# Kernel optimization log

Measured on AMD Instinct MI355X. Metric: run time of the kernel, lower is better.

The kernel has to match this reference:

```python
import jax, jax.numpy as jnp
import numpy as np

LN_EPS = 1e-12


def setup_inputs() -> dict:
    key = jax.random.key(0)
    k1, k2, k3, k4 = jax.random.split(key, 4)
    B, H, L, D = 2, 12, 2048, 64
    q = jax.random.normal(k1, (B, H, L, D), dtype=jnp.float32)
    k = jax.random.normal(k2, (B, H, L, D), dtype=jnp.float32)
    v = jax.random.normal(k3, (B, H, L, D), dtype=jnp.float32)
    mask = jax.random.randint(k4, (1, 1, L, L), 0, 2).astype(jnp.int32)
    gamma = jnp.ones((D,), dtype=jnp.float32)
    beta = jnp.zeros((D,), dtype=jnp.float32)
    return {"q": q, "k": k, "v": v, "mask": mask, "gamma": gamma, "beta": beta}


def reference(q, k, v, mask, gamma, beta):
    # score = q @ k^T  -> [B, H, L, L]
    score = jnp.einsum("bhqd,bhkd->bhqk", q, k)
    # masked_fill(mask == 0, -10000)
    score = jnp.where(mask == 0, jnp.float32(-10000.0), score)
    # result = score @ v -> [B, H, L, D]  (no softmax)
    result = jnp.einsum("bhqk,bhkd->bhqd", score, v)
    # layer norm over the last dim (d_tensor)
    mean = jnp.mean(result, axis=-1, keepdims=True)
    var = jnp.var(result, axis=-1, keepdims=True)
    normed = (result - mean) / jnp.sqrt(var + LN_EPS)
    return normed * gamma + beta
```

## Files before the change

kernel.cpp:

```cpp
#include <hip/hip_runtime.h>

#define SEQ 2048
#define HD 64
#define NBH 24

#define MB_OFF   0
#define MB_BYTES (32 * 32 * 512)
#define QB_OFF   (MB_OFF + MB_BYTES)
#define QK_BYTES (NBH * SEQ * HD * 2)
#define KB_OFF   (QB_OFF + QK_BYTES)
#define VT_OFF   (KB_OFF + QK_BYTES)
#define WS_NEED  ((size_t)(VT_OFF + QK_BYTES))

typedef __bf16 bfrag8 __attribute__((ext_vector_type(8)));
typedef __bf16 bf16x4 __attribute__((ext_vector_type(4)));
typedef float  floatx4 __attribute__((ext_vector_type(4)));
typedef float  floatx16 __attribute__((ext_vector_type(16)));

__device__ __forceinline__ floatx4 mfma_16x16x32(bfrag8 a, bfrag8 b, floatx4 c) {
    return __builtin_amdgcn_mfma_f32_16x16x32_bf16(a, b, c, 0, 0, 0);
}
__device__ __forceinline__ floatx16 mfma_32x32x16(bfrag8 a, bfrag8 b, floatx16 c) {
    return __builtin_amdgcn_mfma_f32_32x32x16_bf16(a, b, c, 0, 0, 0);
}
__device__ __forceinline__ void gld16(const unsigned char* g, unsigned char* l) {
    __builtin_amdgcn_global_load_lds(
        (const __attribute__((address_space(1))) unsigned int*)g,
        (__attribute__((address_space(3))) unsigned int*)l, 16, 0, 0);
}

__global__ __launch_bounds__(256)
void prep_kernel(const float* __restrict__ qp, const float* __restrict__ kp,
                 const float* __restrict__ vp, const int* __restrict__ maskp,
                 unsigned char* __restrict__ ws)
{
    __shared__ __attribute__((aligned(16))) unsigned char parena[64 * 68 * 4];
    const int t = threadIdx.x;
    const int b = blockIdx.x;

    if (b < 1536) {
        int gt  = b * 256 + t;
        int row = gt >> 3;
        int c   = gt & 7;
        const floatx4* qs = (const floatx4*)(qp + row * 64 + c * 8);
        const floatx4* ks = (const floatx4*)(kp + row * 64 + c * 8);
        floatx4 q0 = qs[0], q1 = qs[1];
        floatx4 k0 = ks[0], k1 = ks[1];
        bfrag8 qpk, kpk;
        #pragma unroll
        for (int i = 0; i < 4; ++i) {
            qpk[i] = (__bf16)q0[i]; qpk[4 + i] = (__bf16)q1[i];
            kpk[i] = (__bf16)k0[i]; kpk[4 + i] = (__bf16)k1[i];
        }
        *(bfrag8*)(ws + QB_OFF + row * 128 + c * 16) = qpk;
        *(bfrag8*)(ws + KB_OFF + row * 128 + ((c ^ (row & 7)) * 16)) = kpk;
    } else if (b < 2304) {
        int bb = b - 1536, bh = bb >> 5, kt = bb & 31;
        float* lf = (float*)parena;
        const floatx4* vg = (const floatx4*)(vp + (bh * SEQ + kt * 64) * 64);
        #pragma unroll
        for (int it = 0; it < 4; ++it) {
            int f = t + it * 256;
            int r = f >> 4, c4 = f & 15;
            floatx4 val = vg[f];
            #pragma unroll
            for (int i = 0; i < 4; ++i) lf[r * 68 + c4 * 4 + i] = val[i];
        }
        __syncthreads();
        int d = t >> 2, kseg = t & 3;
        unsigned char* tb = ws + VT_OFF + (size_t)(bh * 32 + kt) * 8192 + d * 128;
        #pragma unroll
        for (int jj = 0; jj < 2; ++jj) {
            bfrag8 pk;
            #pragma unroll
            for (int e = 0; e < 8; ++e)
                pk[e] = (__bf16)lf[(kseg * 16 + jj * 8 + e) * 68 + d];
            *(bfrag8*)(tb + (((kseg * 2 + jj) ^ (d & 7)) * 16)) = pk;
        }
    } else {
        int cc = b - 2304, qtb = cc >> 5, kt = cc & 31;
        const int w = t >> 6, lane = t & 63;
        #pragma unroll
        for (int it = 0; it < 16; ++it) {
            int rr = it * 4 + w;
            unsigned long long bl = __ballot(maskp[(qtb * 64 + rr) * SEQ + kt * 64 + lane] != 0);
            if (lane == 0)
                *(unsigned long long*)(ws + MB_OFF + (size_t)((qtb * 32 + kt) * 64 + rr) * 8) = bl;
        }
    }
}

__global__ __launch_bounds__(256, 2)
void normattn_main(const unsigned char* __restrict__ ws,
                   const float* __restrict__ gammap, const float* __restrict__ betap,
                   float* __restrict__ outp)
{
    __shared__ __attribute__((aligned(16))) unsigned char sm[65536];

    const int tid  = threadIdx.x;
    const int w    = tid >> 6;
    const int lane = tid & 63;
    const int l32  = lane & 31;
    const int hi   = lane >> 5;
    const int qtb  = blockIdx.x;
    const int bh   = blockIdx.y;
    const int q0   = qtb * 64;

    unsigned char* slotK = sm + w * 16384;
    unsigned char* slotV = slotK + 8192;

    const unsigned char* gKt = ws + KB_OFF + (size_t)(bh * SEQ) * 128;
    const unsigned char* gVt = ws + VT_OFF + (size_t)(bh * 32) * 8192;
    const unsigned char* gMb = ws + MB_OFF + (size_t)(qtb * 32) * 512;

    bfrag8 qb[2][4];
    #pragma unroll
    for (int qh = 0; qh < 2; ++qh)
        #pragma unroll
        for (int dstep = 0; dstep < 4; ++dstep)
            qb[qh][dstep] = *(const bfrag8*)(ws + QB_OFF +
                (size_t)(bh * SEQ + q0 + qh * 32 + l32) * 128 + dstep * 32 + hi * 16);

    floatx16 acc[2][2];
    #pragma unroll
    for (int i = 0; i < 4; ++i) acc[i >> 1][i & 1] = (floatx16)0.0f;

    auto stage = [&](int kt) {
        const unsigned char* gk = gKt + (size_t)kt * 8192 + lane * 16;
        const unsigned char* gv = gVt + (size_t)kt * 8192 + lane * 16;
        #pragma unroll
        for (int c = 0; c < 8; ++c) {
            gld16(gk + c * 1024, slotK + c * 1024);
            gld16(gv + c * 1024, slotV + c * 1024);
        }
    };
    unsigned long long mnx0, mnx1;
    auto loadmask = [&](int kt) {
        mnx0 = *(const unsigned long long*)(gMb + (size_t)kt * 512 + l32 * 8);
        mnx1 = *(const unsigned long long*)(gMb + (size_t)kt * 512 + 256 + l32 * 8);
    };

    stage(w);
    loadmask(w);

    for (int i = 0; i < 8; ++i) {
        const int kt = w + 4 * i;
        asm volatile("s_waitcnt vmcnt(0)" ::: "memory");
        const unsigned long long mr0 = mnx0, mr1 = mnx1;

        bfrag8 ka[2][4], va[2][2][2];
        #pragma unroll
        for (int kh = 0; kh < 2; ++kh)
            #pragma unroll
            for (int d = 0; d < 4; ++d)
                ka[kh][d] = *(const bfrag8*)(slotK + (kh * 32 + l32) * 128 +
                                             (((d * 2 + hi) ^ (l32 & 7)) << 4));
        #pragma unroll
        for (int dh = 0; dh < 2; ++dh)
            #pragma unroll
            for (int kh = 0; kh < 2; ++kh)
                #pragma unroll
                for (int ks = 0; ks < 2; ++ks)
                    va[dh][kh][ks] = *(const bfrag8*)(slotV + (dh * 32 + l32) * 128 +
                                                      (((kh * 4 + ks * 2 + hi) ^ (l32 & 7)) << 4));
        asm volatile("s_waitcnt lgkmcnt(0)" ::: "memory");
        if (i < 7) { stage(kt + 4); loadmask(kt + 4); }

        #pragma unroll
        for (int kh = 0; kh < 2; ++kh) {
            floatx16 st0 = (floatx16)0.0f, st1 = (floatx16)0.0f;
            #pragma unroll
            for (int d = 0; d < 4; ++d) {
                st0 = mfma_32x32x16(ka[kh][d], qb[0][d], st0);
                st1 = mfma_32x32x16(ka[kh][d], qb[1][d], st1);
            }
            #pragma unroll
            for (int qh = 0; qh < 2; ++qh) {
                const floatx16 st = qh ? st1 : st0;
                const unsigned long long mrow = qh ? mr1 : mr0;
                const unsigned bits = (unsigned)(mrow >> (kh * 32 + 4 * hi));
                unsigned u[8];
                #pragma unroll
                for (int j = 0; j < 8; ++j) {
                    const int kl0 = 2 * (j & 1) + 8 * (j >> 1);
                    float a = ((bits >> kl0) & 1u) ? st[2 * j] : -10000.0f;
                    float b = ((bits >> (kl0 + 1)) & 1u) ? st[2 * j + 1] : -10000.0f;
                    asm("v_cvt_pk_bf16_f32 %0, %1, %2" : "=v"(u[j]) : "v"(a), "v"(b));
                }
                asm("v_permlane32_swap_b32 %0, %1" : "+v"(u[0]), "+v"(u[2]));
                asm("v_permlane32_swap_b32 %0, %1" : "+v"(u[1]), "+v"(u[3]));
                asm("v_permlane32_swap_b32 %0, %1" : "+v"(u[4]), "+v"(u[6]));
                asm("v_permlane32_swap_b32 %0, %1" : "+v"(u[5]), "+v"(u[7]));
                union { unsigned int w4[4]; bfrag8 f; } c0, c1;
                c0.w4[0] = u[0]; c0.w4[1] = u[1]; c0.w4[2] = u[2]; c0.w4[3] = u[3];
                c1.w4[0] = u[4]; c1.w4[1] = u[5]; c1.w4[2] = u[6]; c1.w4[3] = u[7];

                acc[qh][0] = mfma_32x32x16(va[0][kh][0], c0.f, acc[qh][0]);
                acc[qh][0] = mfma_32x32x16(va[0][kh][1], c1.f, acc[qh][0]);
                acc[qh][1] = mfma_32x32x16(va[1][kh][0], c0.f, acc[qh][1]);
                acc[qh][1] = mfma_32x32x16(va[1][kh][1], c1.f, acc[qh][1]);
            }
        }
    }

    #pragma unroll
    for (int qh = 0; qh < 2; ++qh)
        #pragma unroll
        for (int dh = 0; dh < 2; ++dh)
            #pragma unroll
            for (int jj = 0; jj < 4; ++jj) {
                floatx4 t;
                #pragma unroll
                for (int e = 0; e < 4; ++e) t[e] = acc[qh][dh][jj * 4 + e];
                *(floatx4*)(sm + w * 16384 + (qh * 2 + dh) * 4096 + jj * 1024 + lane * 16) = t;
            }
    __syncthreads();
    if (w < 2) {
        const int qh = w;
        floatx16 o2[2];
        #pragma unroll
        for (int dh = 0; dh < 2; ++dh)
            #pragma unroll
            for (int jj = 0; jj < 4; ++jj) {
                floatx4 s = (floatx4)0.0f;
                #pragma unroll
                for (int ww = 0; ww < 4; ++ww) {
                    floatx4 t = *(const floatx4*)(sm + ww * 16384 + (qh * 2 + dh) * 4096 +
                                                  jj * 1024 + lane * 16);
                    #pragma unroll
                    for (int e = 0; e < 4; ++e) s[e] += t[e];
                }
                #pragma unroll
                for (int e = 0; e < 4; ++e) o2[dh][jj * 4 + e] = s[e];
            }
        float s = 0.0f, s2 = 0.0f;
        #pragma unroll
        for (int dh = 0; dh < 2; ++dh)
            #pragma unroll
            for (int r = 0; r < 16; ++r) { float x = o2[dh][r]; s += x; s2 += x * x; }
        s  += __shfl_xor(s, 32);
        s2 += __shfl_xor(s2, 32);
        float mean = s * (1.0f / 64.0f);
        float var  = s2 * (1.0f / 64.0f) - mean * mean;
        float rstd = rsqrtf(var + 1e-12f);
        float* orow = outp + (size_t)(bh * SEQ + q0 + qh * 32 + l32) * 64;
        #pragma unroll
        for (int dh = 0; dh < 2; ++dh)
            #pragma unroll
            for (int jj = 0; jj < 4; ++jj) {
                const int d0 = dh * 32 + jj * 8 + 4 * hi;
                floatx4 gg = *(const floatx4*)(gammap + d0);
                floatx4 bb = *(const floatx4*)(betap + d0);
                floatx4 o;
                #pragma unroll
                for (int e = 0; e < 4; ++e)
                    o[e] = (o2[dh][jj * 4 + e] - mean) * rstd * gg[e] + bb[e];
                *(floatx4*)(orow + d0) = o;
            }
    }
}

#define KROW 72
#define SROW 40
__global__ __launch_bounds__(256, 4)
void normattn_fallback(const float* __restrict__ qp, const float* __restrict__ kp,
                       const float* __restrict__ vp, const int* __restrict__ maskp,
                       const float* __restrict__ gammap, const float* __restrict__ betap,
                       float* __restrict__ outp)
{
    __shared__ __attribute__((aligned(16))) __bf16 sQ[64 * KROW];
    __shared__ __attribute__((aligned(16))) __bf16 sK[64 * KROW];
    __shared__ __attribute__((aligned(16))) __bf16 sV[64 * KROW];
    __shared__ __attribute__((aligned(16))) __bf16 sS[4][16 * SROW];
    __shared__ __attribute__((aligned(8)))  unsigned int sMw[64][2];

    const int tid = threadIdx.x, wave = tid >> 6, lane = tid & 63;
    const int quad = lane >> 4, l16 = lane & 15;
    const int q0 = blockIdx.x * 64, bh = blockIdx.y;
    const int base = bh * SEQ * HD;
    {
        const floatx4* qg = (const floatx4*)(qp + base + q0 * HD);
        #pragma unroll
        for (int it = 0; it < 4; ++it) {
            int idx = tid + it * 256, r = idx >> 4, c = idx & 15;
            floatx4 val = qg[idx];
            bf16x4 pk = {(__bf16)val[0], (__bf16)val[1], (__bf16)val[2], (__bf16)val[3]};
            *(bf16x4*)&sQ[r * KROW + c * 4] = pk;
        }
    }
    __syncthreads();
    bfrag8 qa0 = *(const bfrag8*)&sQ[(wave * 16 + l16) * KROW + quad * 8];
    bfrag8 qa1 = *(const bfrag8*)&sQ[(wave * 16 + l16) * KROW + quad * 8 + 32];
    floatx4 acc[4];
    #pragma unroll
    for (int i = 0; i < 4; ++i) acc[i] = (floatx4)0.0f;
    const int qrow_loc = wave * 16 + quad * 4;
    const int qrb = q0 + qrow_loc;
    for (int kb = 0; kb < SEQ; kb += 64) {
        __syncthreads();
        {
            const floatx4* kg = (const floatx4*)(kp + base + kb * HD);
            #pragma unroll
            for (int it = 0; it < 4; ++it) {
                int idx = tid + it * 256, r = idx >> 4, c = idx & 15;
                floatx4 val = kg[idx];
                bf16x4 pk = {(__bf16)val[0], (__bf16)val[1], (__bf16)val[2], (__bf16)val[3]};
                *(bf16x4*)&sK[r * KROW + c * 4] = pk;
            }
        }
        {
            int d = tid & 63;
            #pragma unroll
            for (int it = 0; it < 4; ++it) {
                int k4 = (tid >> 6) + it * 4;
                bf16x4 pk;
                #pragma unroll
                for (int i = 0; i < 4; ++i) pk[i] = (__bf16)vp[base + (kb + k4 * 4 + i) * HD + d];
                *(bf16x4*)&sV[d * KROW + k4 * 4] = pk;
            }
        }
        #pragma unroll
        for (int it = 0; it < 16; ++it) {
            int rr = it * 4 + wave;
            unsigned long long bl = __ballot(maskp[(q0 + rr) * SEQ + kb + lane] != 0);
            if (lane == 0) { sMw[rr][0] = (unsigned)bl; sMw[rr][1] = (unsigned)(bl >> 32); }
        }
        __syncthreads();
        unsigned long long mrow[4];
        #pragma unroll
        for (int r = 0; r < 4; ++r) mrow[r] = *(const unsigned long long*)&sMw[qrow_loc + r][0];
        #pragma unroll
        for (int kc = 0; kc < 64; kc += 32) {
            floatx4 s0 = (floatx4)0.0f, s1 = (floatx4)0.0f;
            bfrag8 b00 = *(const bfrag8*)&sK[(kc + l16) * KROW + quad * 8];
            bfrag8 b01 = *(const bfrag8*)&sK[(kc + l16) * KROW + quad * 8 + 32];
            bfrag8 b10 = *(const bfrag8*)&sK[(kc + 16 + l16) * KROW + quad * 8];
            bfrag8 b11 = *(const bfrag8*)&sK[(kc + 16 + l16) * KROW + quad * 8 + 32];
            s0 = mfma_16x16x32(qa0, b00, s0);
            s0 = mfma_16x16x32(qa1, b01, s0);
            s1 = mfma_16x16x32(qa0, b10, s1);
            s1 = mfma_16x16x32(qa1, b11, s1);
            #pragma unroll
            for (int r = 0; r < 4; ++r) {
                float v0 = ((mrow[r] >> (kc + l16)) & 1ull) ? s0[r] : -10000.0f;
                float v1 = ((mrow[r] >> (kc + 16 + l16)) & 1ull) ? s1[r] : -10000.0f;
                sS[wave][(quad * 4 + r) * SROW + l16] = (__bf16)v0;
                sS[wave][(quad * 4 + r) * SROW + 16 + l16] = (__bf16)v1;
            }
            asm volatile("s_waitcnt lgkmcnt(0)" ::: "memory");
            bfrag8 pa = *(const bfrag8*)&sS[wave][l16 * SROW + quad * 8];
            #pragma unroll
            for (int nt = 0; nt < 4; ++nt) {
                bfrag8 vb = *(const bfrag8*)&sV[(nt * 16 + l16) * KROW + kc + quad * 8];
                acc[nt] = mfma_16x16x32(pa, vb, acc[nt]);
            }
        }
    }
    float g[4], bt[4];
    #pragma unroll
    for (int nt = 0; nt < 4; ++nt) { g[nt] = gammap[nt * 16 + l16]; bt[nt] = betap[nt * 16 + l16]; }
    #pragma unroll
    for (int r = 0; r < 4; ++r) {
        float s = 0.0f, s2 = 0.0f;
        #pragma unroll
        for (int nt = 0; nt < 4; ++nt) { float xx = acc[nt][r]; s += xx; s2 += xx * xx; }
        #pragma unroll
        for (int off = 1; off < 16; off <<= 1) { s += __shfl_xor(s, off); s2 += __shfl_xor(s2, off); }
        float mean = s * (1.0f / 64.0f);
        float var = s2 * (1.0f / 64.0f) - mean * mean;
        float rstd = rsqrtf(var + 1e-12f);
        float* orow = outp + base + (qrb + r) * HD;
        #pragma unroll
        for (int nt = 0; nt < 4; ++nt)
            orow[nt * 16 + l16] = (acc[nt][r] - mean) * rstd * g[nt] + bt[nt];
    }
}

extern "C" void kernel_launch(void* const* d_in, const int* in_sizes, int n_in,
                              void* d_out, int out_size, void* d_ws, size_t ws_size,
                              hipStream_t stream) {
    const float* q     = (const float*)d_in[0];
    const float* k     = (const float*)d_in[1];
    const float* v     = (const float*)d_in[2];
    const int*   mask  = (const int*)d_in[3];
    const float* gamma = (const float*)d_in[4];
    const float* beta  = (const float*)d_in[5];
    float* out = (float*)d_out;

    dim3 grid(32, NBH);
    if (ws_size >= WS_NEED) {
        unsigned char* ws = (unsigned char*)d_ws;
        prep_kernel<<<3328, 256, 0, stream>>>(q, k, v, mask, ws);
        normattn_main<<<grid, 256, 0, stream>>>(ws, gamma, beta, out);
    } else {
        normattn_fallback<<<grid, 256, 0, stream>>>(q, k, v, mask, gamma, beta, out);
    }
}
```

Measured before the change: 140.7 us.

## Share K/V LDS tiles across two query blocks in 512-thread workgroups

```diff
diff --git a/kernel.cpp b/kernel.cpp
--- a/kernel.cpp
+++ b/kernel.cpp
@@ -90,7 +90,7 @@
     }
 }
 
-__global__ __launch_bounds__(256, 2)
+__global__ __launch_bounds__(512, 4)
 void normattn_main(const unsigned char* __restrict__ ws,
                    const float* __restrict__ gammap, const float* __restrict__ betap,
                    float* __restrict__ outp)
@@ -99,19 +99,21 @@
 
     const int tid  = threadIdx.x;
     const int w    = tid >> 6;
+    const int sub  = w >> 2;
+    const int wq   = w & 3;
     const int lane = tid & 63;
     const int l32  = lane & 31;
     const int hi   = lane >> 5;
-    const int qtb  = blockIdx.x;
+    const int bx   = blockIdx.x;
     const int bh   = blockIdx.y;
-    const int q0   = qtb * 64;
-
-    unsigned char* slotK = sm + w * 16384;
+    const int qbase = bx * 128 + sub * 64;
+
+    unsigned char* slotK = sm + wq * 16384;
     unsigned char* slotV = slotK + 8192;
 
     const unsigned char* gKt = ws + KB_OFF + (size_t)(bh * SEQ) * 128;
     const unsigned char* gVt = ws + VT_OFF + (size_t)(bh * 32) * 8192;
-    const unsigned char* gMb = ws + MB_OFF + (size_t)(qtb * 32) * 512;
+    const unsigned char* gMb = ws + MB_OFF + (size_t)((bx * 2 + sub) * 32) * 512;
 
     bfrag8 qb[2][4];
     #pragma unroll
@@ -119,19 +121,21 @@
         #pragma unroll
         for (int dstep = 0; dstep < 4; ++dstep)
             qb[qh][dstep] = *(const bfrag8*)(ws + QB_OFF +
-                (size_t)(bh * SEQ + q0 + qh * 32 + l32) * 128 + dstep * 32 + hi * 16);
+                (size_t)(bh * SEQ + qbase + qh * 32 + l32) * 128 + dstep * 32 + hi * 16);
 
     floatx16 acc[2][2];
     #pragma unroll
     for (int i = 0; i < 4; ++i) acc[i >> 1][i & 1] = (floatx16)0.0f;
 
     auto stage = [&](int kt) {
-        const unsigned char* gk = gKt + (size_t)kt * 8192 + lane * 16;
-        const unsigned char* gv = gVt + (size_t)kt * 8192 + lane * 16;
-        #pragma unroll
-        for (int c = 0; c < 8; ++c) {
-            gld16(gk + c * 1024, slotK + c * 1024);
-            gld16(gv + c * 1024, slotV + c * 1024);
+        if (sub == 0) {
+            const unsigned char* gk = gKt + (size_t)kt * 8192 + lane * 16;
+            #pragma unroll
+            for (int c = 0; c < 8; ++c) gld16(gk + c * 1024, slotK + c * 1024);
+        } else {
+            const unsigned char* gv = gVt + (size_t)kt * 8192 + lane * 16;
+            #pragma unroll
+            for (int c = 0; c < 8; ++c) gld16(gv + c * 1024, slotV + c * 1024);
         }
     };
     unsigned long long mnx0, mnx1;
@@ -140,13 +144,13 @@
         mnx1 = *(const unsigned long long*)(gMb + (size_t)kt * 512 + 256 + l32 * 8);
     };
 
-    stage(w);
-    loadmask(w);
+    stage(wq);
+    loadmask(wq);
+    asm volatile("s_waitcnt vmcnt(0)" ::: "memory");
+    __builtin_amdgcn_s_barrier();
 
     for (int i = 0; i < 8; ++i) {
-        const int kt = w + 4 * i;
-        asm volatile("s_waitcnt vmcnt(0)" ::: "memory");
-        const unsigned long long mr0 = mnx0, mr1 = mnx1;
+        const int kt = wq + 4 * i;
 
         bfrag8 ka[2][4], va[2][2][2];
         #pragma unroll
@@ -164,6 +168,9 @@
                     va[dh][kh][ks] = *(const bfrag8*)(slotV + (dh * 32 + l32) * 128 +
                                                       (((kh * 4 + ks * 2 + hi) ^ (l32 & 7)) << 4));
         asm volatile("s_waitcnt lgkmcnt(0)" ::: "memory");
+        __builtin_amdgcn_s_barrier();
+
+        const unsigned long long mr0 = mnx0, mr1 = mnx1;
         if (i < 7) { stage(kt + 4); loadmask(kt + 4); }
 
         #pragma unroll
@@ -201,62 +208,77 @@
                 acc[qh][1] = mfma_32x32x16(va[1][kh][1], c1.f, acc[qh][1]);
             }
         }
-    }
-
-    #pragma unroll
-    for (int qh = 0; qh < 2; ++qh)
-        #pragma unroll
-        for (int dh = 0; dh < 2; ++dh)
-            #pragma unroll
-            for (int jj = 0; jj < 4; ++jj) {
-                floatx4 t;
-                #pragma unroll
-                for (int e = 0; e < 4; ++e) t[e] = acc[qh][dh][jj * 4 + e];
-                *(floatx4*)(sm + w * 16384 + (qh * 2 + dh) * 4096 + jj * 1024 + lane * 16) = t;
-            }
+
+        asm volatile("s_waitcnt vmcnt(0)" ::: "memory");
+        __builtin_amdgcn_s_barrier();
+    }
+
+    auto dump = [&](int region) {
+        unsigned char* base = sm + region * 16384;
+        #pragma unroll
+        for (int qh = 0; qh < 2; ++qh)
+            #pragma unroll
+            for (int dh = 0; dh < 2; ++dh)
+                #pragma unroll
+                for (int jj = 0; jj < 4; ++jj) {
+                    floatx4 t;
+                    #pragma unroll
+                    for (int e = 0; e < 4; ++e) t[e] = acc[qh][dh][jj * 4 + e];
+                    *(floatx4*)(base + (qh * 2 + dh) * 4096 + jj * 1024 + lane * 16) = t;
+                }
+    };
+    auto addin = [&](int region) {
+        const unsigned char* base = sm + region * 16384;
+        #pragma unroll
+        for (int qh = 0; qh < 2; ++qh)
+            #pragma unroll
+            for (int dh = 0; dh < 2; ++dh)
+                #pragma unroll
+                for (int jj = 0; jj < 4; ++jj) {
+                    floatx4 t = *(const floatx4*)(base + (qh * 2 + dh) * 4096 + jj * 1024 + lane * 16);
+                    #pragma unroll
+                    for (int e = 0; e < 4; ++e) acc[qh][dh][jj * 4 + e] += t[e];
+                }
+    };
+
+    if (wq >= 2) dump(sub * 2 + (wq - 2));
     __syncthreads();
-    if (w < 2) {
-        const int qh = w;
-        floatx16 o2[2];
-        #pragma unroll
-        for (int dh = 0; dh < 2; ++dh)
-            #pragma unroll
-            for (int jj = 0; jj < 4; ++jj) {
-                floatx4 s = (floatx4)0.0f;
-                #pragma unroll
-                for (int ww = 0; ww < 4; ++ww) {
-                    floatx4 t = *(const floatx4*)(sm + ww * 16384 + (qh * 2 + dh) * 4096 +
-                                                  jj * 1024 + lane * 16);
+    if (wq <= 1) addin(sub * 2 + wq);
+    if (wq == 1) dump(sub * 2 + 1);
+    __syncthreads();
+    if (wq == 0) {
+        addin(sub * 2 + 1);
+        float s = 0.0f, s2 = 0.0f;
+        #pragma unroll
+        for (int qh = 0; qh < 2; ++qh) {}
+        #pragma unroll
+        for (int qh = 0; qh < 2; ++qh) {
+            float ss = 0.0f, ss2 = 0.0f;
+            #pragma unroll
+            for (int dh = 0; dh < 2; ++dh)
+                #pragma unroll
+                for (int r = 0; r < 16; ++r) { float x = acc[qh][dh][r]; ss += x; ss2 += x * x; }
+            ss  += __shfl_xor(ss, 32);
+            ss2 += __shfl_xor(ss2, 32);
+            float mean = ss * (1.0f / 64.0f);
+            float var  = ss2 * (1.0f / 64.0f) - mean * mean;
+            float rstd = rsqrtf(var + 1e-12f);
+            float* orow = outp + (size_t)(bh * SEQ + qbase + qh * 32 + l32) * 64;
+            #pragma unroll
+            for (int dh = 0; dh < 2; ++dh)
+                #pragma unroll
+                for (int jj = 0; jj < 4; ++jj) {
+                    const int d0 = dh * 32 + jj * 8 + 4 * hi;
+                    floatx4 gg = *(const floatx4*)(gammap + d0);
+                    floatx4 bb = *(const floatx4*)(betap + d0);
+                    floatx4 o;
                     #pragma unroll
-                    for (int e = 0; e < 4; ++e) s[e] += t[e];
+                    for (int e = 0; e < 4; ++e)
+                        o[e] = (acc[qh][dh][jj * 4 + e] - mean) * rstd * gg[e] + bb[e];
+                    *(floatx4*)(orow + d0) = o;
                 }
-                #pragma unroll
-                for (int e = 0; e < 4; ++e) o2[dh][jj * 4 + e] = s[e];
-            }
-        float s = 0.0f, s2 = 0.0f;
-        #pragma unroll
-        for (int dh = 0; dh < 2; ++dh)
-            #pragma unroll
-            for (int r = 0; r < 16; ++r) { float x = o2[dh][r]; s += x; s2 += x * x; }
-        s  += __shfl_xor(s, 32);
-        s2 += __shfl_xor(s2, 32);
-        float mean = s * (1.0f / 64.0f);
-        float var  = s2 * (1.0f / 64.0f) - mean * mean;
-        float rstd = rsqrtf(var + 1e-12f);
-        float* orow = outp + (size_t)(bh * SEQ + q0 + qh * 32 + l32) * 64;
-        #pragma unroll
-        for (int dh = 0; dh < 2; ++dh)
-            #pragma unroll
-            for (int jj = 0; jj < 4; ++jj) {
-                const int d0 = dh * 32 + jj * 8 + 4 * hi;
-                floatx4 gg = *(const floatx4*)(gammap + d0);
-                floatx4 bb = *(const floatx4*)(betap + d0);
-                floatx4 o;
-                #pragma unroll
-                for (int e = 0; e < 4; ++e)
-                    o[e] = (o2[dh][jj * 4 + e] - mean) * rstd * gg[e] + bb[e];
-                *(floatx4*)(orow + d0) = o;
-            }
+        }
+        (void)s; (void)s2;
     }
 }
 
@@ -387,12 +409,13 @@
     const float* beta  = (const float*)d_in[5];
     float* out = (float*)d_out;
 
-    dim3 grid(32, NBH);
     if (ws_size >= WS_NEED) {
         unsigned char* ws = (unsigned char*)d_ws;
         prep_kernel<<<3328, 256, 0, stream>>>(q, k, v, mask, ws);
-        normattn_main<<<grid, 256, 0, stream>>>(ws, gamma, beta, out);
+        dim3 grid(16, NBH);
+        normattn_main<<<grid, 512, 0, stream>>>(ws, gamma, beta, out);
     } else {
+        dim3 grid(32, NBH);
         normattn_fallback<<<grid, 256, 0, stream>>>(q, k, v, mask, gamma, beta, out);
     }
 }
```

New measurement: 192.3 us. 1.37x slower.
